# Kernel optimization log

Measured on AMD Instinct MI355X. Metric: run time of the kernel, lower is better.

The kernel has to match this reference:

```python
import jax, jax.numpy as jnp
import numpy as np

EPS = 1e-5
K = 20
LRELU = 0.2


def _bn(x, g, b, ch_axis):
    # inference BatchNorm with running_mean=0, running_var=1
    shape = [1] * x.ndim
    shape[ch_axis] = -1
    scale = (g / jnp.sqrt(1.0 + EPS)).reshape(shape)
    bias = b.reshape(shape)
    return x * scale + bias


def _lrelu(x):
    return jnp.where(x > 0, x, LRELU * x)


def _edge_conv(x, W, g, b):
    # x: (B, C, N) -> (B, C_out, N)
    B, C, N = x.shape
    xt = jnp.swapaxes(x, 1, 2)                      # (B, N, C)
    inner = -2.0 * jnp.einsum('bnc,bmc->bnm', xt, xt)
    xx = jnp.sum(xt * xt, axis=2)                   # (B, N)
    pdist = -xx[:, :, None] - inner - xx[:, None, :]  # negative sq dist (B,N,N)
    idx = jax.lax.top_k(pdist, K)[1]                # (B, N, K) nearest (incl. self)
    # gather neighbor features per batch: (C, N) indexed by (N, K) -> (C, N, K)
    neighbors = jax.vmap(lambda xf, id_: xf[:, id_])(x, idx)  # (B, C, N, K)
    center = jnp.broadcast_to(x[..., None], (B, C, N, K))
    edge = jnp.concatenate([center, neighbors - center], axis=1)  # (B, 2C, N, K)
    h = jnp.einsum('oc,bcnk->bonk', W, edge)        # 1x1 conv, no bias
    h = _lrelu(_bn(h, g, b, 1))
    return jnp.max(h, axis=-1)                      # (B, C_out, N)


def setup_inputs() -> dict:
    key = jax.random.key(0)
    ks = jax.random.split(key, 24)
    B, N = 4, 2048
    d = {}
    d['points'] = jax.random.normal(ks[0], (B, N, 3), dtype=jnp.float32)

    def w(k_, shape):
        return 0.1 * jax.random.normal(k_, shape, dtype=jnp.float32)

    def gam(k_, c):
        return 1.0 + 0.1 * jax.random.normal(k_, (c,), dtype=jnp.float32)

    def bet(k_, c):
        return 0.05 * jax.random.normal(k_, (c,), dtype=jnp.float32)

    # EdgeConv blocks: (out, 2*in)
    d['w1'], d['g1'], d['b1'] = w(ks[1], (64, 6)), gam(ks[2], 64), bet(ks[3], 64)
    d['w2'], d['g2'], d['b2'] = w(ks[4], (64, 128)), gam(ks[5], 64), bet(ks[6], 64)
    d['w3'], d['g3'], d['b3'] = w(ks[7], (128, 128)), gam(ks[8], 128), bet(ks[9], 128)
    d['w4'], d['g4'], d['b4'] = w(ks[10], (256, 256)), gam(ks[11], 256), bet(ks[12], 256)
    # conv5 1x1: 512 -> 1024
    d['w5'], d['g5'], d['b5'] = w(ks[13], (1024, 512)), gam(ks[14], 1024), bet(ks[15], 1024)
    # fc: 2048 -> 512 -> 256
    d['fw1'], d['fb1'] = w(ks[16], (512, 2048)), 0.05 * jax.random.normal(ks[17], (512,), dtype=jnp.float32)
    d['g6'], d['b6'] = gam(ks[18], 512), bet(ks[19], 512)
    d['fw2'], d['fb2'] = w(ks[20], (256, 512)), 0.05 * jax.random.normal(ks[21], (256,), dtype=jnp.float32)
    d['g7'], d['b7'] = gam(ks[22], 256), bet(ks[23], 256)
    return d


def reference(points, w1, g1, b1, w2, g2, b2, w3, g3, b3, w4, g4, b4,
              w5, g5, b5, fw1, fb1, g6, b6, fw2, fb2, g7, b7):
    x = jnp.swapaxes(points[:, :, :3], 1, 2)        # (B, 3, N)
    x1 = _edge_conv(x, w1, g1, b1)                  # (B, 64, N)
    x2 = _edge_conv(x1, w2, g2, b2)                 # (B, 64, N)
    x3 = _edge_conv(x2, w3, g3, b3)                 # (B, 128, N)
    x4 = _edge_conv(x3, w4, g4, b4)                 # (B, 256, N)
    h = jnp.concatenate([x1, x2, x3, x4], axis=1)   # (B, 512, N)
    h = _lrelu(_bn(jnp.einsum('oc,bcn->bon', w5, h), g5, b5, 1))  # (B, 1024, N)
    h_max = jnp.max(h, axis=-1)
    h_avg = jnp.mean(h, axis=-1)
    f = jnp.concatenate([h_max, h_avg], axis=1)     # (B, 2048)
    f = _lrelu(_bn(f @ fw1.T + fb1, g6, b6, 1))     # dropout = identity (eval)
    f = _bn(f @ fw2.T + fb2, g7, b7, 1)
    return f                                        # (B, 256)
```

## Files before the change

kernel.cpp:

```cpp
#include <hip/hip_runtime.h>
#include <hip/hip_bf16.h>
#include <float.h>

#define N_PTS 2048
#define B_SZ  4
#define KNN   20
#define LRELU_S 0.2f
#define FT    512
#define NPOOL 8

typedef __hip_bfloat16 bf16;
typedef __attribute__((ext_vector_type(8))) short short8v;
typedef __attribute__((ext_vector_type(4))) float floatx4;

__device__ __forceinline__ float b2f(const bf16 v) { return __bfloat162float(v); }
__device__ __forceinline__ float ldf(const float* p) { return *p; }
__device__ __forceinline__ float ldf(const bf16* p)  { return __bfloat162float(*p); }
__device__ __forceinline__ short8v ld8(const bf16* p) { return *(const short8v*)p; }
__device__ __forceinline__ unsigned umin(unsigned a, unsigned b) { return a < b ? a : b; }

__device__ __forceinline__ void gload16(const void* g, void* l) {
    __builtin_amdgcn_global_load_lds(
        (const __attribute__((address_space(1))) void*)g,
        (__attribute__((address_space(3))) void*)l, 16, 0, 0);
}

__global__ void k_sniff(const unsigned short* __restrict__ pts_hw, int* __restrict__ flag) {
    if (threadIdx.x != 0 || blockIdx.x != 0) return;
    int sane = 0;
    for (int j = 0; j < 64; ++j) {
        unsigned short v = pts_hw[2 * j];
        int e = (v >> 7) & 0xFF;
        if (e >= 100 && e <= 140) ++sane;
    }
    *flag = (sane >= 32) ? 1 : 0;
}

struct WPack {
    const void* src[23];
    int off[24];
    int rows[23];
    int cols[23];
};

__device__ __forceinline__ void repack_body(const WPack& wp, int isb,
                                            float* __restrict__ dst, int i, int limit) {
    if (i >= limit) return;
    int lo = 0, hi = 23;
    while (lo + 1 < hi) { int mid = (lo + hi) >> 1; if (i >= wp.off[mid]) lo = mid; else hi = mid; }
    int j = i - wp.off[lo];
    float v = isb ? b2f(((const bf16*)wp.src[lo])[j]) : ((const float*)wp.src[lo])[j];
    int dj = j;
    int cols = wp.cols[lo];
    if (cols) dj = (j % cols) * wp.rows[lo] + (j / cols);
    dst[wp.off[lo] + dj] = v;
}

template<int C, int COUT>
__device__ __forceinline__ void wsplit_body(const void* __restrict__ W, int isb,
                                            bf16* __restrict__ dst, int i) {
    if (i >= COUT * C) return;
    int o = i / C, c = i % C;
    float w1 = isb ? b2f(((const bf16*)W)[(size_t)o * 2 * C + c])
                   : ((const float*)W)[(size_t)o * 2 * C + c];
    float w2 = isb ? b2f(((const bf16*)W)[(size_t)o * 2 * C + C + c])
                   : ((const float*)W)[(size_t)o * 2 * C + C + c];
    float wd = w1 - w2;
    bf16 h2 = __float2bfloat16(w2);
    bf16 hd = __float2bfloat16(wd);
    dst[i]                = h2;
    dst[COUT * C + i]     = __float2bfloat16(w2 - b2f(h2));
    dst[2 * COUT * C + i] = hd;
    dst[3 * COUT * C + i] = __float2bfloat16(wd - b2f(hd));
}

__device__ __forceinline__ void w5split_body(const void* __restrict__ W, int isb,
                                             bf16* __restrict__ dst, int i) {
    if (i >= 1024 * 512) return;
    float w = isb ? b2f(((const bf16*)W)[i]) : ((const float*)W)[i];
    bf16 h = __float2bfloat16(w);
    dst[i] = h;
    dst[1024 * 512 + i] = __float2bfloat16(w - b2f(h));
}

__device__ __forceinline__ void transpose_body(const void* __restrict__ pts, int isb,
                                               float* __restrict__ x0, int i) {
    if (i >= B_SZ * N_PTS) return;
    int b = i / N_PTS, n = i % N_PTS;
    for (int c = 0; c < 3; ++c) {
        size_t s = ((size_t)b * N_PTS + n) * 3 + c;
        float v = isb ? b2f(((const bf16*)pts)[s]) : ((const float*)pts)[s];
        x0[((size_t)b * 3 + c) * N_PTS + n] = v;
    }
}

__global__ void k_prep(WPack wp, const int* __restrict__ flag, float* __restrict__ wf,
                       int rlimit,
                       const void* __restrict__ w2s, bf16* __restrict__ wsp2,
                       const void* __restrict__ w3s, bf16* __restrict__ wsp3,
                       const void* __restrict__ w4s, bf16* __restrict__ wsp4,
                       const void* __restrict__ w5s, bf16* __restrict__ w5sp,
                       const void* __restrict__ pts, float* __restrict__ x0) {
    const int isb = *flag;
    const int nbrep = (rlimit + 255) >> 8;
    int ib = blockIdx.x, t = threadIdx.x;
    if (ib < nbrep) { repack_body(wp, isb, wf, ib * 256 + t, rlimit); return; }
    ib -= nbrep;
    if (ib < 16)   { wsplit_body<64, 64>(w2s, isb, wsp2, ib * 256 + t); return; }
    ib -= 16;
    if (ib < 32)   { wsplit_body<64, 128>(w3s, isb, wsp3, ib * 256 + t); return; }
    ib -= 32;
    if (ib < 128)  { wsplit_body<128, 256>(w4s, isb, wsp4, ib * 256 + t); return; }
    ib -= 128;
    if (ib < 2048) { w5split_body(w5s, isb, w5sp, ib * 256 + t); return; }
    ib -= 2048;
    transpose_body(pts, isb, x0, ib * 256 + t);
}

__global__ void k_repack(WPack wp, const int* __restrict__ flag, float* __restrict__ dst, int limit) {
    repack_body(wp, *flag, dst, blockIdx.x * blockDim.x + threadIdx.x, limit);
}
__global__ void k_transpose(const void* __restrict__ pts, const int* __restrict__ flag,
                            float* __restrict__ x0) {
    transpose_body(pts, *flag, x0, blockIdx.x * blockDim.x + threadIdx.x);
}

__device__ __forceinline__ void load32(const float* row, int mbase, float* r) {
    const float4* p = (const float4*)(row + mbase);
#pragma unroll
    for (int i = 0; i < 8; ++i) {
        float4 f = p[i];
        r[4 * i + 0] = f.x; r[4 * i + 1] = f.y; r[4 * i + 2] = f.z; r[4 * i + 3] = f.w;
    }
}
__device__ __forceinline__ void load32(const bf16* row, int mbase, float* r) {
    const uint4* p = (const uint4*)(row + mbase);
// ... 67 lines not shown
        int q = threadIdx.x / 3, c = threadIdx.x % 3;
        qf[q][c] = xb[(size_t)c * N_PTS + q0 + q];
    }
    __syncthreads();

    int w = threadIdx.x >> 6, lane = threadIdx.x & 63;
    int qa = q0 + 2 * w;
    int mbase = lane * 32;

    float da[32], db[32];
#pragma unroll
    for (int j = 0; j < 32; ++j) { da[j] = 0.f; db[j] = 0.f; }
#pragma unroll
    for (int c = 0; c < 3; ++c) {
        float r[32];
        load32(xb + (size_t)c * N_PTS, mbase, r);
        float qac = qf[2 * w][c], qbc = qf[2 * w + 1][c];
#pragma unroll
        for (int j = 0; j < 32; ++j) {
            float ta = r[j] - qac; da[j] = fmaf(ta, ta, da[j]);
            float tb = r[j] - qbc; db[j] = fmaf(tb, tb, db[j]);
        }
    }
    unsigned ka[32], kb[32];
#pragma unroll
    for (int j = 0; j < 32; ++j) {
        ka[j] = (__float_as_uint(da[j]) & 0xFFFFF800u) | (unsigned)(mbase + j);
        kb[j] = (__float_as_uint(db[j]) & 0xFFFFF800u) | (unsigned)(mbase + j);
    }
    select20x2(ka, kb, idx + ((size_t)b * N_PTS + qa) * KNN,
               idx + ((size_t)b * N_PTS + qa + 1) * KNN, lane);
}

__global__ __launch_bounds__(256) void k_select2(const float* __restrict__ G,
                                                 const float* __restrict__ xx,
                                                 int* __restrict__ idx) {
    int ib = blockIdx.x;
    int b  = ib / (N_PTS / 8);
    int q0 = (ib % (N_PTS / 8)) * 8;
    int w = threadIdx.x >> 6, lane = threadIdx.x & 63;
    int qa = q0 + 2 * w;
    const float* gA = G + ((size_t)b * N_PTS + qa) * N_PTS;
    const float* gB = gA + N_PTS;
    const float* xr = xx + (size_t)b * N_PTS;
    float xqa = xr[qa], xqb = xr[qa + 1];

    unsigned ka[32], kb[32];
#pragma unroll
    for (int r = 0; r < 8; ++r) {
        int m0 = r * 256 + (lane << 2);
        float4 x4 = *(const float4*)(xr + m0);
        float4 a4 = *(const float4*)(gA + m0);
        float4 b4 = *(const float4*)(gB + m0);
        float s;
        s = fmaf(-2.f, a4.x, x4.x) + xqa; s = fmaxf(s, 0.f);
        ka[4 * r + 0] = (__float_as_uint(s) & 0xFFFFF800u) | (unsigned)(m0 + 0);
        s = fmaf(-2.f, a4.y, x4.y) + xqa; s = fmaxf(s, 0.f);
        ka[4 * r + 1] = (__float_as_uint(s) & 0xFFFFF800u) | (unsigned)(m0 + 1);
        s = fmaf(-2.f, a4.z, x4.z) + xqa; s = fmaxf(s, 0.f);
        ka[4 * r + 2] = (__float_as_uint(s) & 0xFFFFF800u) | (unsigned)(m0 + 2);
        s = fmaf(-2.f, a4.w, x4.w) + xqa; s = fmaxf(s, 0.f);
        ka[4 * r + 3] = (__float_as_uint(s) & 0xFFFFF800u) | (unsigned)(m0 + 3);
        s = fmaf(-2.f, b4.x, x4.x) + xqb; s = fmaxf(s, 0.f);
        kb[4 * r + 0] = (__float_as_uint(s) & 0xFFFFF800u) | (unsigned)(m0 + 0);
        s = fmaf(-2.f, b4.y, x4.y) + xqb; s = fmaxf(s, 0.f);
        kb[4 * r + 1] = (__float_as_uint(s) & 0xFFFFF800u) | (unsigned)(m0 + 1);
        s = fmaf(-2.f, b4.z, x4.z) + xqb; s = fmaxf(s, 0.f);
        kb[4 * r + 2] = (__float_as_uint(s) & 0xFFFFF800u) | (unsigned)(m0 + 2);
        s = fmaf(-2.f, b4.w, x4.w) + xqb; s = fmaxf(s, 0.f);
        kb[4 * r + 3] = (__float_as_uint(s) & 0xFFFFF800u) | (unsigned)(m0 + 3);
    }
    select20x2(ka, kb, idx + ((size_t)b * N_PTS + qa) * KNN,
               idx + ((size_t)b * N_PTS + qa + 1) * KNN, lane);
}

template<typename T, int C>
__global__ __launch_bounds__(256) void k_knn(const T* __restrict__ x, int bstride,
                                             int* __restrict__ idx) {
    __shared__ float qf[4][C];
    int ib = blockIdx.x;
    int b  = ib / (N_PTS / 4);
    int q0 = (ib % (N_PTS / 4)) * 4;
    const T* xb = x + (size_t)b * bstride;

    for (int t = threadIdx.x; t < 4 * C; t += 256) {
        int pt = t / C, c = t % C;
        qf[pt][c] = ldf(&xb[(size_t)c * N_PTS + (q0 + pt)]);
    }
    __syncthreads();

    int w = threadIdx.x >> 6, lane = threadIdx.x & 63;
    int q = q0 + w;
    int mbase = lane * 32;

    float v[32];
#pragma unroll
    for (int j = 0; j < 32; ++j) v[j] = 0.f;

    for (int c = 0; c < C; ++c) {
        float qc = qf[w][c];
        float r[32];
        load32(xb + (size_t)c * N_PTS, mbase, r);
#pragma unroll
        for (int j = 0; j < 32; ++j) { float t = r[j] - qc; v[j] = fmaf(t, t, v[j]); }
    }

    for (int k = 0; k < KNN; ++k) {
        float bv = FLT_MAX; int bi = 0x7FFFFFFF;
#pragma unroll
        for (int j = 0; j < 32; ++j)
            if (v[j] < bv) { bv = v[j]; bi = mbase + j; }
#pragma unroll
        for (int off = 32; off >= 1; off >>= 1) {
            float ov = __shfl_xor(bv, off);
            int   oi = __shfl_xor(bi, off);
            if (ov < bv || (ov == bv && oi < bi)) { bv = ov; bi = oi; }
        }
        if (lane == 0) idx[((size_t)b * N_PTS + q) * KNN + k] = bi;
        int wl = bi >> 5, wj = bi & 31;
        if (lane == wl) {
#pragma unroll
            for (int j = 0; j < 32; ++j) if (j == wj) v[j] = FLT_MAX;
        }
    }
}

template<int C>
__global__ __launch_bounds__(256) void k_gram(const bf16* __restrict__ featT, int c0,
                                              float* __restrict__ G) {
    const int KC = 64;
    __shared__ __align__(16) short At[128 * 64];
    __shared__ __align__(16) short Bt[128 * 64];

    int ib = blockIdx.x;
    int b  = ib >> 8;
    int t  = ib & 255;
    int n0 = (t >> 4) << 7;
    int m0 = (t & 15) << 7;

    int tid = threadIdx.x;
    int w = tid >> 6, lane = tid & 63;
    int rw = (w & 1) * 64, cw = (w >> 1) * 64;
    int lrow = lane & 15, quad = lane >> 4;

    floatx4 acc[4][4];
#pragma unroll
    for (int ri = 0; ri < 4; ++ri)
#pragma unroll
        for (int ci = 0; ci < 4; ++ci) acc[ri][ci] = (floatx4){0.f, 0.f, 0.f, 0.f};

    for (int ck = 0; ck < C; ck += KC) {
        __syncthreads();
#pragma unroll
        for (int it = 0; it < 4; ++it) {
            int s = tid + it * 256;
            int row = s >> 3, seg = s & 7;
            int gseg = seg ^ (row & 7);
            gload16(featT + ((size_t)(b * N_PTS + n0 + row) * FT) + c0 + ck + gseg * 8,
                    &At[(s & ~63) * 8]);
            gload16(featT + ((size_t)(b * N_PTS + m0 + row) * FT) + c0 + ck + gseg * 8,
                    &Bt[(s & ~63) * 8]);
        }
        __syncthreads();
#pragma unroll
        for (int kk = 0; kk < KC; kk += 32) {
            int ks = kk >> 3;
            short8v a[4], bb[4];
#pragma unroll
            for (int ri = 0; ri < 4; ++ri) {
                int row = rw + ri * 16 + lrow;
                int seg = (ks + quad) ^ (row & 7);
                a[ri] = *(const short8v*)&At[row * 64 + seg * 8];
            }
#pragma unroll
            for (int ci = 0; ci < 4; ++ci) {
                int row = cw + ci * 16 + lrow;
                int seg = (ks + quad) ^ (row & 7);
                bb[ci] = *(const short8v*)&Bt[row * 64 + seg * 8];
            }
#pragma unroll
            for (int ri = 0; ri < 4; ++ri)
#pragma unroll
                for (int ci = 0; ci < 4; ++ci)
                    acc[ri][ci] = __builtin_amdgcn_mfma_f32_16x16x32_bf16(a[ri], bb[ci], acc[ri][ci], 0, 0, 0);
        }
    }

#pragma unroll
    for (int ri = 0; ri < 4; ++ri)
#pragma unroll
        for (int ci = 0; ci < 4; ++ci) {
            int n = n0 + rw + ri * 16 + quad * 4;
            int m = m0 + cw + ci * 16 + lrow;
            float* gp = G + ((size_t)b * N_PTS + n) * N_PTS + m;
#pragma unroll
            for (int reg = 0; reg < 4; ++reg)
                gp[(size_t)reg * N_PTS] = acc[ri][ci][reg];
        }
}

template<int COUT, int C>
__global__ __launch_bounds__(256) void k_xform(const bf16* __restrict__ featT, int c0,
                                               const bf16* __restrict__ Wsp,
                                               float* __restrict__ Y,
                                               const int* __restrict__ flag) {
    const int M2 = 2 * COUT;
    const int KC = 64;
    __shared__ __align__(16) short Bt[128 * 64];

    const int isb = *flag;
    int ib = blockIdx.x;
    int nt = ib & 63;
    int mt = ib >> 6;
    int tid = threadIdx.x;
    int w = tid >> 6, lane = tid & 63;
    int rw = (w & 1) * 64, cw = (w >> 1) * 64;
    int l15 = lane & 15, quad = lane >> 4;

    floatx4 acc[4][4];
#pragma unroll
    for (int ri = 0; ri < 4; ++ri)
#pragma unroll
        for (int ci = 0; ci < 4; ++ci) acc[ri][ci] = (floatx4){0.f, 0.f, 0.f, 0.f};

    for (int ck = 0; ck < C; ck += KC) {
        __syncthreads();
#pragma unroll
        for (int it = 0; it < 4; ++it) {
            int s = tid + it * 256;
            int row = s >> 3, seg = s & 7;
            int gseg = seg ^ (row & 7);
            gload16(featT + (size_t)(nt * 128 + row) * FT + c0 + ck + gseg * 8,
                    &Bt[(s & ~63) * 8]);
        }
        __syncthreads();
#pragma unroll
        for (int kk = 0; kk < KC; kk += 32) {
            int ks = kk >> 3;
            short8v bfr[4];
#pragma unroll
            for (int ci = 0; ci < 4; ++ci) {
                int row = cw + ci * 16 + l15;
                int seg = (ks + quad) ^ (row & 7);
                bfr[ci] = *(const short8v*)&Bt[row * 64 + seg * 8];
            }
#pragma unroll
            for (int ri = 0; ri < 4; ++ri) {
                int rbase = mt * 128 + rw + ri * 16;
                bool uselo = (!isb) || (rbase >= COUT);
                int mrow = rbase + l15;
                int base = (mrow < COUT) ? mrow : (mrow + COUT);
                const bf16* hi = Wsp + (size_t)base * C + ck + kk + quad * 8;
                short8v ah = ld8(hi);
                short8v al;
                if (uselo) al = ld8(hi + (size_t)COUT * C);
#pragma unroll
                for (int ci = 0; ci < 4; ++ci) {
                    acc[ri][ci] = __builtin_amdgcn_mfma_f32_16x16x32_bf16(ah, bfr[ci], acc[ri][ci], 0, 0, 0);
                    if (uselo)
                        acc[ri][ci] = __builtin_amdgcn_mfma_f32_16x16x32_bf16(al, bfr[ci], acc[ri][ci], 0, 0, 0);
                }
            }
        }
    }

#pragma unroll
    for (int ri = 0; ri < 4; ++ri)
#pragma unroll
        for (int ci = 0; ci < 4; ++ci) {
            int n = nt * 128 + cw + ci * 16 + l15;
            int m = mt * 128 + rw + ri * 16 + quad * 4;
            *(floatx4*)(Y + (size_t)n * M2 + m) = acc[ri][ci];
        }
}

template<int COUT>
__global__ __launch_bounds__(256) void k_gmax(const float* __restrict__ Y,
        const int* __restrict__ idx,
        const float* __restrict__ gam, const float* __restrict__ bet,
        bf16* __restrict__ featT, int c0f, float* __restrict__ xxout) {
    const int M2 = 2 * COUT;
    const int OT = COUT / 64;
    int i = blockIdx.x * 4 + (threadIdx.x >> 6);
    int lane = threadIdx.x & 63;
    int b = i >> 11;

    const float inv = rsqrtf(1.0f + 1e-5f);
    float yd[OT], scale[OT], bias[OT], mx[OT];
#pragma unroll
    for (int j = 0; j < OT; ++j) {
        int o = lane + 64 * j;
        yd[j]    = Y[(size_t)i * M2 + COUT + o];
        scale[j] = gam[o] * inv;
        bias[j]  = bet[o];
        mx[j]    = -FLT_MAX;
    }

    const int* ip = idx + (size_t)i * KNN;
    const float* Yb = Y + ((size_t)b * N_PTS) * M2;
#pragma unroll 4
    for (int k = 0; k < KNN; ++k) {
        int m = ip[k] & (N_PTS - 1);
        const float* yr = Yb + (size_t)m * M2;
#pragma unroll
        for (int j = 0; j < OT; ++j) {
            float h = (yd[j] + yr[lane + 64 * j]) * scale[j] + bias[j];
            h = h > 0.f ? h : LRELU_S * h;
            mx[j] = fmaxf(mx[j], h);
        }
    }
    float s = 0.f;
#pragma unroll
    for (int j = 0; j < OT; ++j) {
        bf16 bv = __float2bfloat16(mx[j]);
        featT[(size_t)i * FT + c0f + lane + 64 * j] = bv;
        if (xxout) { float q = b2f(bv); s = fmaf(q, q, s); }
    }
    if (xxout) {
#pragma unroll
        for (int off = 32; off >= 1; off >>= 1) s += __shfl_xor(s, off);
        if (lane == 0) xxout[i] = s;
    }
}

template<typename T, int C, int COUT, bool WF>
__global__ __launch_bounds__(256) void k_edgeconv(const T* __restrict__ x, int bstride,
                           const int* __restrict__ idx,
                           const float* __restrict__ Wt,
                           const float* __restrict__ gam,
                           const float* __restrict__ bet,
                           bf16* __restrict__ out, int ostride,
                           bf16* __restrict__ featT, int c0f,
                           float* __restrict__ xxout) {
    const int PT = 4;
    const int OT = COUT / 64;
    const int CP = (C + 3) & ~3;
    __shared__ float sh[PT][KNN + 1][CP];

    int ib = blockIdx.x;
    int b  = ib / (N_PTS / PT);
    int n0 = (ib % (N_PTS / PT)) * PT;
    const T* xb = x + (size_t)b * bstride;

    const int TOT = PT * (KNN + 1) * C;
    for (int t = threadIdx.x; t < TOT; t += 256) {
        int pt = t / ((KNN + 1) * C);
        int r  = t % ((KNN + 1) * C);
        int row = r / C, c = r % C;
        int n = n0 + pt;
        int m = (row == 0) ? n
                           : (idx[((size_t)b * N_PTS + n) * KNN + (row - 1)] & (N_PTS - 1));
        sh[pt][row][c] = ldf(&xb[(size_t)c * N_PTS + m]);
    }
    __syncthreads();
// ... 28 lines not shown
            if (pass == 0) {
#pragma unroll
                for (int j = 0; j < OT; ++j) {
                    float w1v = Wt[(size_t)c * COUT + lane + 64 * j];
                    base[j] = fmaf(w1v - w2v[j], xq, base[j]);
                }
            }
#pragma unroll
            for (int k = 0; k < KT; ++k) {
                float nv = sh[w][1 + pass * KT + k][c];
#pragma unroll
                for (int j = 0; j < OT; ++j) acc[j][k] = fmaf(w2v[j], nv, acc[j][k]);
            }
        }

#pragma unroll
        for (int j = 0; j < OT; ++j) {
            int o = lane + 64 * j;
            float scale = gam[o] * inv, bias = bet[o];
#pragma unroll
            for (int k = 0; k < KT; ++k) {
                float h = (base[j] + acc[j][k]) * scale + bias;
                h = h > 0.f ? h : LRELU_S * h;
                mx[j] = fmaxf(mx[j], h);
            }
        }
    }

    float s = 0.f;
#pragma unroll
    for (int j = 0; j < OT; ++j) {
        int o = lane + 64 * j;
        bf16 bv = __float2bfloat16(mx[j]);
        out[(size_t)b * ostride + (size_t)o * N_PTS + n] = bv;
        if (WF) {
            featT[((size_t)b * N_PTS + n) * FT + c0f + o] = bv;
            float q = b2f(bv);
            s = fmaf(q, q, s);
        }
    }
    if (WF && xxout) {
#pragma unroll
        for (int off = 32; off >= 1; off >>= 1) s += __shfl_xor(s, off);
        if (lane == 0) xxout[(size_t)b * N_PTS + n] = s;
    }
}

__global__ __launch_bounds__(256) void k_conv5mfma(
        const bf16* __restrict__ featT, const bf16* __restrict__ w5sp,
        const float* __restrict__ g5, const float* __restrict__ b5,
        float* __restrict__ fmxp, float* __restrict__ fsmp,
        const int* __restrict__ flag) {
    __shared__ __align__(16) short Bt[256 * 64];
    __shared__ __align__(16) short Ah[64 * 64];
    __shared__ __align__(16) short Al[64 * 64];
    __shared__ float rmx[4][64];
    __shared__ float rsm[4][64];

    const int isb = *flag;
    int ib = blockIdx.x;
    int b  = ib / 128;
    int rem = ib % 128;
    int o0 = (rem >> 3) * 64;
    int nt = rem & 7;
    int tid = threadIdx.x;
    int w = tid >> 6, lane = tid & 63;
    int l15 = lane & 15, quad = lane >> 4;
// ... 302 lines not shown
extern "C" void kernel_launch(void* const* d_in, const int* in_sizes, int n_in,
                              void* d_out, int out_size, void* d_ws, size_t ws_size,
                              hipStream_t stream) {
    static const int wsz[23] = {
        384, 64, 64,   8192, 64, 64,   16384, 128, 128,   65536, 256, 256,
        524288, 1024, 1024,   1048576, 512,   512, 512,   131072, 256,   256, 256
    };
    static const int trows[23] = {64,0,0, 64,0,0, 128,0,0, 256,0,0, 0,0,0, 0,0, 0,0, 0,0, 0,0};
    static const int tcols[23] = { 6,0,0,128,0,0, 128,0,0, 256,0,0, 0,0,0, 0,0, 0,0, 0,0, 0,0};

    WPack wp;
    int total = 0;
    for (int i = 0; i < 23; ++i) {
        wp.src[i] = d_in[i + 1]; wp.off[i] = total; total += wsz[i];
        wp.rows[i] = trows[i]; wp.cols[i] = tcols[i];
    }
    wp.off[23] = total;

    const size_t flag_bytes = 16;
    const size_t x0_bytes   = (size_t)B_SZ * 3 * N_PTS * 4;
    const size_t feat_bytes = (size_t)B_SZ * 512 * N_PTS * 2;
    const size_t idx_bytes  = (size_t)B_SZ * N_PTS * KNN * 4;
    const size_t pool_bytes = (size_t)B_SZ * 1024 * 4 * 2;
    const size_t wf_bytes   = (size_t)total * 4;
    const size_t base_need  = flag_bytes + x0_bytes + feat_bytes + idx_bytes + pool_bytes + wf_bytes;

    const size_t featT_bytes = (size_t)B_SZ * N_PTS * FT * 2;
    const size_t xx_bytes    = (size_t)B_SZ * N_PTS * 4;
    const size_t wsp2_elems  = 4 * 64 * 64;
    const size_t wsp3_elems  = 4 * 128 * 64;
    const size_t wsp4_elems  = 4 * 256 * 128;
    const size_t w5sp_elems  = 2 * 1024 * 512;
    const size_t wsp_bytes   = (wsp2_elems + wsp3_elems + wsp4_elems + w5sp_elems) * 2;
    const size_t S_bytes     = (size_t)B_SZ * N_PTS * N_PTS * 4;
    const size_t full_need   = base_need + featT_bytes + xx_bytes + wsp_bytes + S_bytes;

    if (ws_size < base_need) return;
    const bool use_gram = (ws_size >= full_need);

    char* w = (char*)d_ws;
    int*   flag = (int*)w;              w += flag_bytes;
    float* x0   = (float*)w;            w += x0_bytes;
    bf16*  feat = (bf16*)w;             w += feat_bytes;
    int*   idx  = (int*)w;              w += idx_bytes;
    w += pool_bytes;
    float* wf   = (float*)w;            w += wf_bytes;
    bf16*  featT = (bf16*)w;            w += featT_bytes;
    float* xx    = (float*)w;           w += xx_bytes;
    bf16*  wsp2  = (bf16*)w;            w += wsp2_elems * 2;
    bf16*  wsp3  = (bf16*)w;            w += wsp3_elems * 2;
    bf16*  wsp4  = (bf16*)w;            w += wsp4_elems * 2;
    bf16*  w5sp  = (bf16*)w;            w += w5sp_elems * 2;
    float* S     = (float*)w;

    float* fmxp = (float*)idx;
    float* fsmp = fmxp + (size_t)B_SZ * 1024 * NPOOL;
    float* fvec = fsmp + (size_t)B_SZ * 1024 * NPOOL;
    float* tbuf = fvec + (size_t)B_SZ * 2048;

    const int FBS = 512 * N_PTS;

    k_sniff<<<1, 64, 0, stream>>>((const unsigned short*)d_in[0], flag);

    const float* w1t = wf + wp.off[0],  *g1 = wf + wp.off[1],  *b1 = wf + wp.off[2];
    const float* w2t = wf + wp.off[3],  *g2 = wf + wp.off[4],  *b2 = wf + wp.off[5];
    const float* w3t = wf + wp.off[6],  *g3 = wf + wp.off[7],  *b3 = wf + wp.off[8];
    const float* w4t = wf + wp.off[9],  *g4 = wf + wp.off[10], *b4 = wf + wp.off[11];
    const float* w5  = wf + wp.off[12], *g5 = wf + wp.off[13], *b5 = wf + wp.off[14];
    const float* fw1 = wf + wp.off[15], *fb1 = wf + wp.off[16];
    const float* g6  = wf + wp.off[17], *b6 = wf + wp.off[18];
    const float* fw2 = wf + wp.off[19], *fb2 = wf + wp.off[20];
    const float* g7  = wf + wp.off[21], *b7 = wf + wp.off[22];

    const int GK = B_SZ * N_PTS / 4;
    const int G8 = B_SZ * N_PTS / 8;

    if (use_gram) {
        const int rlimit = wp.off[15];
        const int nbrep = (rlimit + 255) / 256;
        const int prep_grid = nbrep + 16 + 32 + 128 + 2048 + 32;
        k_prep<<<prep_grid, 256, 0, stream>>>(wp, flag, wf, rlimit,
                                              d_in[4], wsp2, d_in[7], wsp3,
                                              d_in[10], wsp4, d_in[13], w5sp,
                                              d_in[0], x0);

        k_knn3<<<G8, 256, 0, stream>>>(x0, idx);
        k_edgeconv<float, 3, 64, true><<<GK, 256, 0, stream>>>(
            x0, 3 * N_PTS, idx, w1t, g1, b1, feat + 0 * N_PTS, FBS, featT, 0, xx);
        k_gram<64><<<B_SZ * 256, 256, 0, stream>>>(featT, 0, S);
        k_select2<<<G8, 256, 0, stream>>>(S, xx, idx);
        k_xform<64, 64><<<64, 256, 0, stream>>>(featT, 0, wsp2, S, flag);
        k_gmax<64><<<GK, 256, 0, stream>>>(S, idx, g2, b2, featT, 64, xx);
        k_gram<64><<<B_SZ * 256, 256, 0, stream>>>(featT, 64, S);
        k_select2<<<G8, 256, 0, stream>>>(S, xx, idx);
        k_xform<128, 64><<<128, 256, 0, stream>>>(featT, 64, wsp3, S, flag);
        k_gmax<128><<<GK, 256, 0, stream>>>(S, idx, g3, b3, featT, 128, xx);
        k_gram<128><<<B_SZ * 256, 256, 0, stream>>>(featT, 128, S);
        k_select2<<<G8, 256, 0, stream>>>(S, xx, idx);
        k_xform<256, 128><<<256, 256, 0, stream>>>(featT, 128, wsp4, S, flag);
        k_gmax<256><<<GK, 256, 0, stream>>>(S, idx, g4, b4, featT, 256, nullptr);

        k_conv5mfma<<<B_SZ * 128, 256, 0, stream>>>(featT, w5sp, g5, b5, fmxp, fsmp, flag);
        k_pool<<<(B_SZ * 1024 + 255) / 256, 256, 0, stream>>>(fmxp, fsmp, fvec);
        k_fc1<<<B_SZ * 512, 256, 0, stream>>>(fvec, d_in[16], d_in[17], d_in[18], d_in[19],
                                              flag, tbuf);
        k_fc2<<<B_SZ * 256, 256, 0, stream>>>(tbuf, d_in[20], d_in[21], d_in[22], d_in[23],
                                              flag, d_out);
    } else {
        k_repack<<<(total + 255) / 256, 256, 0, stream>>>(wp, flag, wf, total);
        k_transpose<<<(B_SZ * N_PTS + 255) / 256, 256, 0, stream>>>(d_in[0], flag, x0);

        k_knn<float, 3><<<GK, 256, 0, stream>>>(x0, 3 * N_PTS, idx);
        k_edgeconv<float, 3, 64, false><<<GK, 256, 0, stream>>>(
            x0, 3 * N_PTS, idx, w1t, g1, b1, feat + 0 * N_PTS, FBS, nullptr, 0, nullptr);
        k_knn<bf16, 64><<<GK, 256, 0, stream>>>(feat + 0 * N_PTS, FBS, idx);
        k_edgeconv<bf16, 64, 64, false><<<GK, 256, 0, stream>>>(
            feat + 0 * N_PTS, FBS, idx, w2t, g2, b2, feat + 64 * N_PTS, FBS, nullptr, 0, nullptr);
        k_knn<bf16, 64><<<GK, 256, 0, stream>>>(feat + 64 * N_PTS, FBS, idx);
        k_edgeconv<bf16, 64, 128, false><<<GK, 256, 0, stream>>>(
            feat + 64 * N_PTS, FBS, idx, w3t, g3, b3, feat + 128 * N_PTS, FBS, nullptr, 0, nullptr);
        k_knn<bf16, 128><<<GK, 256, 0, stream>>>(feat + 128 * N_PTS, FBS, idx);
        k_edgeconv<bf16, 128, 256, false><<<GK, 256, 0, stream>>>(
            feat + 128 * N_PTS, FBS, idx, w4t, g4, b4, feat + 256 * N_PTS, FBS, nullptr, 0, nullptr);

        k_conv5pool<<<B_SZ * (1024 / 8) * NCH, 256, 0, stream>>>(feat, w5, g5, b5, fmxp, fsmp);
        k_head<<<B_SZ, 256, 0, stream>>>(fmxp, fsmp, fw1, fb1, g6, b6, fw2, fb2, g7, b7,
                                         flag, d_out);
    }
}
```

Before: 382.2 us.

## Fuse gram with xform and kNN select with neighbor max; store Y in bf16

Each of the three later EdgeConv stages now runs in two launches instead of four. The gram and feature-transform GEMMs share one launch. The top-k selection feeds its neighbor indices through shared memory straight into the gather-max, so the idx buffer is no longer written and read back in global memory. The transformed features Y are stored as bf16 in a separate buffer instead of fp32 in S. This cuts gather traffic but adds rounding error. The sniff kernel is folded into k_prep and edgeconv1 skips its redundant channel-major write, which removes more launches and writes. The xx buffers are double-buffered to avoid read/write hazards.

```diff
diff --git a/kernel.cpp b/kernel.cpp
--- a/kernel.cpp
+++ b/kernel.cpp
@@ -11,6 +11,7 @@
 
 typedef __hip_bfloat16 bf16;
 typedef __attribute__((ext_vector_type(8))) short short8v;
+typedef __attribute__((ext_vector_type(4))) short short4v;
 typedef __attribute__((ext_vector_type(4))) float floatx4;
 
 __device__ __forceinline__ float b2f(const bf16 v) { return __bfloat162float(v); }
@@ -18,6 +19,10 @@
 __device__ __forceinline__ float ldf(const bf16* p)  { return __bfloat162float(*p); }
 __device__ __forceinline__ short8v ld8(const bf16* p) { return *(const short8v*)p; }
 __device__ __forceinline__ unsigned umin(unsigned a, unsigned b) { return a < b ? a : b; }
+__device__ __forceinline__ short bfbits(float f) {
+    bf16 t = __float2bfloat16(f);
+    return *reinterpret_cast<short*>(&t);
+}
 
 __device__ __forceinline__ void gload16(const void* g, void* l) {
     __builtin_amdgcn_global_load_lds(
@@ -25,15 +30,19 @@
         (__attribute__((address_space(3))) void*)l, 16, 0, 0);
 }
 
-__global__ void k_sniff(const unsigned short* __restrict__ pts_hw, int* __restrict__ flag) {
-    if (threadIdx.x != 0 || blockIdx.x != 0) return;
+__device__ __forceinline__ int sniff_body(const unsigned short* pts_hw) {
     int sane = 0;
     for (int j = 0; j < 64; ++j) {
         unsigned short v = pts_hw[2 * j];
         int e = (v >> 7) & 0xFF;
         if (e >= 100 && e <= 140) ++sane;
     }
-    *flag = (sane >= 32) ? 1 : 0;
+    return (sane >= 32) ? 1 : 0;
+}
+
+__global__ void k_sniff(const unsigned short* __restrict__ pts_hw, int* __restrict__ flag) {
+    if (threadIdx.x != 0 || blockIdx.x != 0) return;
+    *flag = sniff_body(pts_hw);
 }
 
 struct WPack {
@@ -94,14 +103,21 @@
     }
 }
 
-__global__ void k_prep(WPack wp, const int* __restrict__ flag, float* __restrict__ wf,
-                       int rlimit,
+__global__ void k_prep(WPack wp, float* __restrict__ wf, int rlimit,
                        const void* __restrict__ w2s, bf16* __restrict__ wsp2,
                        const void* __restrict__ w3s, bf16* __restrict__ wsp3,
                        const void* __restrict__ w4s, bf16* __restrict__ wsp4,
                        const void* __restrict__ w5s, bf16* __restrict__ w5sp,
-                       const void* __restrict__ pts, float* __restrict__ x0) {
-    const int isb = *flag;
+                       const void* __restrict__ pts, float* __restrict__ x0,
+                       int* __restrict__ flagout) {
+    __shared__ int sfl;
+    if (threadIdx.x == 0) {
+        int f = sniff_body((const unsigned short*)pts);
+        sfl = f;
+        if (blockIdx.x == 0) *flagout = f;
+    }
+    __syncthreads();
+    const int isb = sfl;
     const int nbrep = (rlimit + 255) >> 8;
     int ib = blockIdx.x, t = threadIdx.x;
     if (ib < nbrep) { repack_body(wp, isb, wf, ib * 256 + t, rlimit); return; }
@@ -235,9 +251,226 @@
                idx + ((size_t)b * N_PTS + qa + 1) * KNN, lane);
 }
 
-__global__ __launch_bounds__(256) void k_select2(const float* __restrict__ G,
-                                                 const float* __restrict__ xx,
-                                                 int* __restrict__ idx) {
+template<typename T, int C>
+__global__ __launch_bounds__(256) void k_knn(const T* __restrict__ x, int bstride,
+                                             int* __restrict__ idx) {
+    __shared__ float qf[4][C];
+    int ib = blockIdx.x;
+    int b  = ib / (N_PTS / 4);
+    int q0 = (ib % (N_PTS / 4)) * 4;
+    const T* xb = x + (size_t)b * bstride;
+
+    for (int t = threadIdx.x; t < 4 * C; t += 256) {
+        int pt = t / C, c = t % C;
+        qf[pt][c] = ldf(&xb[(size_t)c * N_PTS + (q0 + pt)]);
+    }
+    __syncthreads();
+
+    int w = threadIdx.x >> 6, lane = threadIdx.x & 63;
+    int q = q0 + w;
+    int mbase = lane * 32;
+
+    float v[32];
+#pragma unroll
+    for (int j = 0; j < 32; ++j) v[j] = 0.f;
+
+    for (int c = 0; c < C; ++c) {
+        float qc = qf[w][c];
+        float r[32];
+        load32(xb + (size_t)c * N_PTS, mbase, r);
+#pragma unroll
+        for (int j = 0; j < 32; ++j) { float t = r[j] - qc; v[j] = fmaf(t, t, v[j]); }
+    }
+
+    for (int k = 0; k < KNN; ++k) {
+        float bv = FLT_MAX; int bi = 0x7FFFFFFF;
+#pragma unroll
+        for (int j = 0; j < 32; ++j)
+            if (v[j] < bv) { bv = v[j]; bi = mbase + j; }
+#pragma unroll
+        for (int off = 32; off >= 1; off >>= 1) {
+            float ov = __shfl_xor(bv, off);
+            int   oi = __shfl_xor(bi, off);
+            if (ov < bv || (ov == bv && oi < bi)) { bv = ov; bi = oi; }
+        }
+        if (lane == 0) idx[((size_t)b * N_PTS + q) * KNN + k] = bi;
+        int wl = bi >> 5, wj = bi & 31;
+        if (lane == wl) {
+#pragma unroll
+            for (int j = 0; j < 32; ++j) if (j == wj) v[j] = FLT_MAX;
+        }
+    }
+}
+
+template<int C>
+__device__ __forceinline__ void gram_body(const bf16* __restrict__ featT, int c0,
+                                          float* __restrict__ G,
+                                          short* At, short* Bt, int ib) {
+    const int KC = 64;
+    int b  = ib >> 8;
+    int t  = ib & 255;
+    int n0 = (t >> 4) << 7;
+    int m0 = (t & 15) << 7;
+
+    int tid = threadIdx.x;
+    int w = tid >> 6, lane = tid & 63;
+    int rw = (w & 1) * 64, cw = (w >> 1) * 64;
+    int lrow = lane & 15, quad = lane >> 4;
+
+    floatx4 acc[4][4];
+#pragma unroll
+    for (int ri = 0; ri < 4; ++ri)
+#pragma unroll
+        for (int ci = 0; ci < 4; ++ci) acc[ri][ci] = (floatx4){0.f, 0.f, 0.f, 0.f};
+
+    for (int ck = 0; ck < C; ck += KC) {
+        __syncthreads();
+#pragma unroll
+        for (int it = 0; it < 4; ++it) {
+            int s = tid + it * 256;
+            int row = s >> 3, seg = s & 7;
+            int gseg = seg ^ (row & 7);
+            gload16(featT + ((size_t)(b * N_PTS + n0 + row) * FT) + c0 + ck + gseg * 8,
+                    &At[(s & ~63) * 8]);
+            gload16(featT + ((size_t)(b * N_PTS + m0 + row) * FT) + c0 + ck + gseg * 8,
+                    &Bt[(s & ~63) * 8]);
+        }
+        __syncthreads();
+#pragma unroll
+        for (int kk = 0; kk < KC; kk += 32) {
+            int ks = kk >> 3;
+            short8v a[4], bb[4];
+#pragma unroll
+            for (int ri = 0; ri < 4; ++ri) {
+                int row = rw + ri * 16 + lrow;
+                int seg = (ks + quad) ^ (row & 7);
+                a[ri] = *(const short8v*)&At[row * 64 + seg * 8];
+            }
+#pragma unroll
+            for (int ci = 0; ci < 4; ++ci) {
+                int row = cw + ci * 16 + lrow;
+                int seg = (ks + quad) ^ (row & 7);
+                bb[ci] = *(const short8v*)&Bt[row * 64 + seg * 8];
+            }
+#pragma unroll
+            for (int ri = 0; ri < 4; ++ri)
+#pragma unroll
+                for (int ci = 0; ci < 4; ++ci)
+                    acc[ri][ci] = __builtin_amdgcn_mfma_f32_16x16x32_bf16(a[ri], bb[ci], acc[ri][ci], 0, 0, 0);
+        }
+    }
+
+#pragma unroll
+    for (int ri = 0; ri < 4; ++ri)
+#pragma unroll
+        for (int ci = 0; ci < 4; ++ci) {
+            int n = n0 + rw + ri * 16 + quad * 4;
+            int m = m0 + cw + ci * 16 + lrow;
+            float* gp = G + ((size_t)b * N_PTS + n) * N_PTS + m;
+#pragma unroll
+            for (int reg = 0; reg < 4; ++reg)
+                gp[(size_t)reg * N_PTS] = acc[ri][ci][reg];
+        }
+}
+
+template<int COUT, int C>
+__device__ __forceinline__ void xform_body(const bf16* __restrict__ featT, int c0,
+                                           const bf16* __restrict__ Wsp,
+                                           bf16* __restrict__ Yh, int isb,
+                                           short* Bt, int ib2) {
+    const int M2 = 2 * COUT;
+    const int KC = 64;
+    int nt = ib2 & 63;
+    int mt = ib2 >> 6;
+    int tid = threadIdx.x;
+    int w = tid >> 6, lane = tid & 63;
+    int rw = (w & 1) * 64, cw = (w >> 1) * 64;
+    int l15 = lane & 15, quad = lane >> 4;
+
+    floatx4 acc[4][4];
+#pragma unroll
+    for (int ri = 0; ri < 4; ++ri)
+#pragma unroll
+        for (int ci = 0; ci < 4; ++ci) acc[ri][ci] = (floatx4){0.f, 0.f, 0.f, 0.f};
+
+    for (int ck = 0; ck < C; ck += KC) {
+        __syncthreads();
+#pragma unroll
+        for (int it = 0; it < 4; ++it) {
+            int s = tid + it * 256;
+            int row = s >> 3, seg = s & 7;
+            int gseg = seg ^ (row & 7);
+            gload16(featT + (size_t)(nt * 128 + row) * FT + c0 + ck + gseg * 8,
+                    &Bt[(s & ~63) * 8]);
+        }
+        __syncthreads();
+#pragma unroll
+        for (int kk = 0; kk < KC; kk += 32) {
+            int ks = kk >> 3;
+            short8v bfr[4];
+#pragma unroll
+            for (int ci = 0; ci < 4; ++ci) {
+                int row = cw + ci * 16 + l15;
+                int seg = (ks + quad) ^ (row & 7);
+                bfr[ci] = *(const short8v*)&Bt[row * 64 + seg * 8];
+            }
+#pragma unroll
+            for (int ri = 0; ri < 4; ++ri) {
+                int rbase = mt * 128 + rw + ri * 16;
+                bool uselo = (!isb) || (rbase >= COUT);
+                int mrow = rbase + l15;
+                int base = (mrow < COUT) ? mrow : (mrow + COUT);
+                const bf16* hi = Wsp + (size_t)base * C + ck + kk + quad * 8;
+                short8v ah = ld8(hi);
+                short8v al;
+                if (uselo) al = ld8(hi + (size_t)COUT * C);
+#pragma unroll
+                for (int ci = 0; ci < 4; ++ci) {
+                    acc[ri][ci] = __builtin_amdgcn_mfma_f32_16x16x32_bf16(ah, bfr[ci], acc[ri][ci], 0, 0, 0);
+                    if (uselo)
+                        acc[ri][ci] = __builtin_amdgcn_mfma_f32_16x16x32_bf16(al, bfr[ci], acc[ri][ci], 0, 0, 0);
+                }
+            }
+        }
+    }
+
+#pragma unroll
+    for (int ri = 0; ri < 4; ++ri)
+#pragma unroll
+        for (int ci = 0; ci < 4; ++ci) {
+            int n = nt * 128 + cw + ci * 16 + l15;
+            int m = mt * 128 + rw + ri * 16 + quad * 4;
+            short4v o4;
+            o4[0] = bfbits(acc[ri][ci][0]);
+            o4[1] = bfbits(acc[ri][ci][1]);
+            o4[2] = bfbits(acc[ri][ci][2]);
+            o4[3] = bfbits(acc[ri][ci][3]);
+            *(short4v*)(Yh + (size_t)n * M2 + m) = o4;
+        }
+}
+
+template<int C, int COUT>
+__global__ __launch_bounds__(256) void k_gx(const bf16* __restrict__ featT, int c0,
+        const bf16* __restrict__ Wsp, float* __restrict__ G, bf16* __restrict__ Yh,
+        const int* __restrict__ flag) {
+    __shared__ __align__(16) short lds[2 * 128 * 64];
+    int ib = blockIdx.x;
+    if (ib < B_SZ * 256) {
+        gram_body<C>(featT, c0, G, lds, lds + 128 * 64, ib);
+    } else {
+        xform_body<COUT, C>(featT, c0, Wsp, Yh, *flag, lds, ib - B_SZ * 256);
+    }
+}
+
+template<int COUT>
+__global__ __launch_bounds__(256) void k_selgmax(const float* __restrict__ G,
+        const float* __restrict__ xxin, const bf16* __restrict__ Yh,
+        const float* __restrict__ gam, const float* __restrict__ bet,
+        bf16* __restrict__ featT, int c0f, float* __restrict__ xxout) {
+    const int M2 = 2 * COUT;
+    const int OT = COUT / 64;
+    __shared__ int sidx[8][KNN];
+
     int ib = blockIdx.x;
     int b  = ib / (N_PTS / 8);
     int q0 = (ib % (N_PTS / 8)) * 8;
@@ -245,7 +478,7 @@
     int qa = q0 + 2 * w;
     const float* gA = G + ((size_t)b * N_PTS + qa) * N_PTS;
     const float* gB = gA + N_PTS;
-    const float* xr = xx + (size_t)b * N_PTS;
+    const float* xr = xxin + (size_t)b * N_PTS;
     float xqa = xr[qa], xqb = xr[qa + 1];
 
     unsigned ka[32], kb[32];
@@ -273,256 +506,58 @@
         s = fmaf(-2.f, b4.w, x4.w) + xqb; s = fmaxf(s, 0.f);
         kb[4 * r + 3] = (__float_as_uint(s) & 0xFFFFF800u) | (unsigned)(m0 + 3);
     }
-    select20x2(ka, kb, idx + ((size_t)b * N_PTS + qa) * KNN,
-               idx + ((size_t)b * N_PTS + qa + 1) * KNN, lane);
-}
-
-template<typename T, int C>
-__global__ __launch_bounds__(256) void k_knn(const T* __restrict__ x, int bstride,
-                                             int* __restrict__ idx) {
-    __shared__ float qf[4][C];
-    int ib = blockIdx.x;
-    int b  = ib / (N_PTS / 4);
-    int q0 = (ib % (N_PTS / 4)) * 4;
-    const T* xb = x + (size_t)b * bstride;
-
-    for (int t = threadIdx.x; t < 4 * C; t += 256) {
-        int pt = t / C, c = t % C;
-        qf[pt][c] = ldf(&xb[(size_t)c * N_PTS + (q0 + pt)]);
-    }
+    select20x2(ka, kb, &sidx[2 * w][0], &sidx[2 * w + 1][0], lane);
     __syncthreads();
 
-    int w = threadIdx.x >> 6, lane = threadIdx.x & 63;
-    int q = q0 + w;
-    int mbase = lane * 32;
-
-    float v[32];
-#pragma unroll
-    for (int j = 0; j < 32; ++j) v[j] = 0.f;
-
-    for (int c = 0; c < C; ++c) {
-        float qc = qf[w][c];
-        float r[32];
-        load32(xb + (size_t)c * N_PTS, mbase, r);
-#pragma unroll
-        for (int j = 0; j < 32; ++j) { float t = r[j] - qc; v[j] = fmaf(t, t, v[j]); }
-    }
-
-    for (int k = 0; k < KNN; ++k) {
-        float bv = FLT_MAX; int bi = 0x7FFFFFFF;
-#pragma unroll
-        for (int j = 0; j < 32; ++j)
-            if (v[j] < bv) { bv = v[j]; bi = mbase + j; }
-#pragma unroll
-        for (int off = 32; off >= 1; off >>= 1) {
-            float ov = __shfl_xor(bv, off);
-            int   oi = __shfl_xor(bi, off);
-            if (ov < bv || (ov == bv && oi < bi)) { bv = ov; bi = oi; }
-        }
-        if (lane == 0) idx[((size_t)b * N_PTS + q) * KNN + k] = bi;
-        int wl = bi >> 5, wj = bi & 31;
-        if (lane == wl) {
-#pragma unroll
-            for (int j = 0; j < 32; ++j) if (j == wj) v[j] = FLT_MAX;
-        }
-    }
-}
-
-template<int C>
-__global__ __launch_bounds__(256) void k_gram(const bf16* __restrict__ featT, int c0,
-                                              float* __restrict__ G) {
-    const int KC = 64;
-    __shared__ __align__(16) short At[128 * 64];
-    __shared__ __align__(16) short Bt[128 * 64];
-
-    int ib = blockIdx.x;
-    int b  = ib >> 8;
-    int t  = ib & 255;
-    int n0 = (t >> 4) << 7;
-    int m0 = (t & 15) << 7;
-
-    int tid = threadIdx.x;
-    int w = tid >> 6, lane = tid & 63;
-    int rw = (w & 1) * 64, cw = (w >> 1) * 64;
-    int lrow = lane & 15, quad = lane >> 4;
-
-    floatx4 acc[4][4];
-#pragma unroll
-    for (int ri = 0; ri < 4; ++ri)
-#pragma unroll
-        for (int ci = 0; ci < 4; ++ci) acc[ri][ci] = (floatx4){0.f, 0.f, 0.f, 0.f};
-
-    for (int ck = 0; ck < C; ck += KC) {
-        __syncthreads();
-#pragma unroll
-        for (int it = 0; it < 4; ++it) {
-            int s = tid + it * 256;
-            int row = s >> 3, seg = s & 7;
-            int gseg = seg ^ (row & 7);
-            gload16(featT + ((size_t)(b * N_PTS + n0 + row) * FT) + c0 + ck + gseg * 8,
-                    &At[(s & ~63) * 8]);
-            gload16(featT + ((size_t)(b * N_PTS + m0 + row) * FT) + c0 + ck + gseg * 8,
-                    &Bt[(s & ~63) * 8]);
-        }
-        __syncthreads();
-#pragma unroll
-        for (int kk = 0; kk < KC; kk += 32) {
-            int ks = kk >> 3;
-            short8v a[4], bb[4];
-#pragma unroll
-            for (int ri = 0; ri < 4; ++ri) {
-                int row = rw + ri * 16 + lrow;
-                int seg = (ks + quad) ^ (row & 7);
-                a[ri] = *(const short8v*)&At[row * 64 + seg * 8];
-            }
-#pragma unroll
-            for (int ci = 0; ci < 4; ++ci) {
-                int row = cw + ci * 16 + lrow;
-                int seg = (ks + quad) ^ (row & 7);
-                bb[ci] = *(const short8v*)&Bt[row * 64 + seg * 8];
-            }
-#pragma unroll
-            for (int ri = 0; ri < 4; ++ri)
-#pragma unroll
-                for (int ci = 0; ci < 4; ++ci)
-                    acc[ri][ci] = __builtin_amdgcn_mfma_f32_16x16x32_bf16(a[ri], bb[ci], acc[ri][ci], 0, 0, 0);
-        }
-    }
-
-#pragma unroll
-    for (int ri = 0; ri < 4; ++ri)
-#pragma unroll
-        for (int ci = 0; ci < 4; ++ci) {
-            int n = n0 + rw + ri * 16 + quad * 4;
-            int m = m0 + cw + ci * 16 + lrow;
-            float* gp = G + ((size_t)b * N_PTS + n) * N_PTS + m;
-#pragma unroll
-            for (int reg = 0; reg < 4; ++reg)
-                gp[(size_t)reg * N_PTS] = acc[ri][ci][reg];
-        }
-}
-
-template<int COUT, int C>
-__global__ __launch_bounds__(256) void k_xform(const bf16* __restrict__ featT, int c0,
-                                               const bf16* __restrict__ Wsp,
-                                               float* __restrict__ Y,
-                                               const int* __restrict__ flag) {
-    const int M2 = 2 * COUT;
-    const int KC = 64;
-    __shared__ __align__(16) short Bt[128 * 64];
-
-    const int isb = *flag;
-    int ib = blockIdx.x;
-    int nt = ib & 63;
-    int mt = ib >> 6;
-    int tid = threadIdx.x;
-    int w = tid >> 6, lane = tid & 63;
-    int rw = (w & 1) * 64, cw = (w >> 1) * 64;
-    int l15 = lane & 15, quad = lane >> 4;
-
-    floatx4 acc[4][4];
-#pragma unroll
-    for (int ri = 0; ri < 4; ++ri)
-#pragma unroll
-        for (int ci = 0; ci < 4; ++ci) acc[ri][ci] = (floatx4){0.f, 0.f, 0.f, 0.f};
-
-    for (int ck = 0; ck < C; ck += KC) {
-        __syncthreads();
-#pragma unroll
-        for (int it = 0; it < 4; ++it) {
-            int s = tid + it * 256;
-            int row = s >> 3, seg = s & 7;
-            int gseg = seg ^ (row & 7);
-            gload16(featT + (size_t)(nt * 128 + row) * FT + c0 + ck + gseg * 8,
-                    &Bt[(s & ~63) * 8]);
-        }
-        __syncthreads();
-#pragma unroll
-        for (int kk = 0; kk < KC; kk += 32) {
-            int ks = kk >> 3;
-            short8v bfr[4];
-#pragma unroll
-            for (int ci = 0; ci < 4; ++ci) {
-                int row = cw + ci * 16 + l15;
-                int seg = (ks + quad) ^ (row & 7);
-                bfr[ci] = *(const short8v*)&Bt[row * 64 + seg * 8];
-            }
-#pragma unroll
-            for (int ri = 0; ri < 4; ++ri) {
-                int rbase = mt * 128 + rw + ri * 16;
-                bool uselo = (!isb) || (rbase >= COUT);
-                int mrow = rbase + l15;
-                int base = (mrow < COUT) ? mrow : (mrow + COUT);
-                const bf16* hi = Wsp + (size_t)base * C + ck + kk + quad * 8;
-                short8v ah = ld8(hi);
-                short8v al;
-                if (uselo) al = ld8(hi + (size_t)COUT * C);
-#pragma unroll
-                for (int ci = 0; ci < 4; ++ci) {
-                    acc[ri][ci] = __builtin_amdgcn_mfma_f32_16x16x32_bf16(ah, bfr[ci], acc[ri][ci], 0, 0, 0);
-                    if (uselo)
-                        acc[ri][ci] = __builtin_amdgcn_mfma_f32_16x16x32_bf16(al, bfr[ci], acc[ri][ci], 0, 0, 0);
-                }
-            }
-        }
-    }
-
-#pragma unroll
-    for (int ri = 0; ri < 4; ++ri)
-#pragma unroll
-        for (int ci = 0; ci < 4; ++ci) {
-            int n = nt * 128 + cw + ci * 16 + l15;
-            int m = mt * 128 + rw + ri * 16 + quad * 4;
-            *(floatx4*)(Y + (size_t)n * M2 + m) = acc[ri][ci];
-        }
-}
-
-template<int COUT>
-__global__ __launch_bounds__(256) void k_gmax(const float* __restrict__ Y,
-        const int* __restrict__ idx,
-        const float* __restrict__ gam, const float* __restrict__ bet,
-        bf16* __restrict__ featT, int c0f, float* __restrict__ xxout) {
-    const int M2 = 2 * COUT;
-    const int OT = COUT / 64;
-    int i = blockIdx.x * 4 + (threadIdx.x >> 6);
-    int lane = threadIdx.x & 63;
-    int b = i >> 11;
-
+    size_t iA = (size_t)b * N_PTS + qa;
     const float inv = rsqrtf(1.0f + 1e-5f);
-    float yd[OT], scale[OT], bias[OT], mx[OT];
+    float yda[OT], ydb[OT], scl[OT], bis[OT], mxa[OT], mxb[OT];
 #pragma unroll
     for (int j = 0; j < OT; ++j) {
         int o = lane + 64 * j;
-        yd[j]    = Y[(size_t)i * M2 + COUT + o];
-        scale[j] = gam[o] * inv;
-        bias[j]  = bet[o];
-        mx[j]    = -FLT_MAX;
-    }
-
-    const int* ip = idx + (size_t)i * KNN;
-    const float* Yb = Y + ((size_t)b * N_PTS) * M2;
-#pragma unroll 4
+        yda[j] = b2f(Yh[iA * M2 + COUT + o]);
+        ydb[j] = b2f(Yh[(iA + 1) * M2 + COUT + o]);
+        scl[j] = gam[o] * inv;
+        bis[j] = bet[o];
+        mxa[j] = -FLT_MAX; mxb[j] = -FLT_MAX;
+    }
+    const bf16* Yb = Yh + (size_t)b * N_PTS * M2;
+#pragma unroll
     for (int k = 0; k < KNN; ++k) {
-        int m = ip[k] & (N_PTS - 1);
-        const float* yr = Yb + (size_t)m * M2;
+        int m0 = sidx[2 * w][k] & (N_PTS - 1);
+        int m1 = sidx[2 * w + 1][k] & (N_PTS - 1);
+        const bf16* r0 = Yb + (size_t)m0 * M2;
+        const bf16* r1 = Yb + (size_t)m1 * M2;
 #pragma unroll
         for (int j = 0; j < OT; ++j) {
-            float h = (yd[j] + yr[lane + 64 * j]) * scale[j] + bias[j];
-            h = h > 0.f ? h : LRELU_S * h;
-            mx[j] = fmaxf(mx[j], h);
-        }
-    }
-    float s = 0.f;
+            int o = lane + 64 * j;
+            float ha = (yda[j] + b2f(r0[o])) * scl[j] + bis[j];
+            ha = ha > 0.f ? ha : LRELU_S * ha;
+            mxa[j] = fmaxf(mxa[j], ha);
+            float hb = (ydb[j] + b2f(r1[o])) * scl[j] + bis[j];
+            hb = hb > 0.f ? hb : LRELU_S * hb;
+            mxb[j] = fmaxf(mxb[j], hb);
+        }
+    }
+    float sa = 0.f, sb = 0.f;
 #pragma unroll
     for (int j = 0; j < OT; ++j) {
-        bf16 bv = __float2bfloat16(mx[j]);
-        featT[(size_t)i * FT + c0f + lane + 64 * j] = bv;
-        if (xxout) { float q = b2f(bv); s = fmaf(q, q, s); }
+        bf16 va = __float2bfloat16(mxa[j]);
+        bf16 vb = __float2bfloat16(mxb[j]);
+        featT[iA * FT + c0f + lane + 64 * j] = va;
+        featT[(iA + 1) * FT + c0f + lane + 64 * j] = vb;
+        if (xxout) {
+            float pa = b2f(va); sa = fmaf(pa, pa, sa);
+            float pb = b2f(vb); sb = fmaf(pb, pb, sb);
+        }
     }
     if (xxout) {
 #pragma unroll
-        for (int off = 32; off >= 1; off >>= 1) s += __shfl_xor(s, off);
-        if (lane == 0) xxout[i] = s;
+        for (int off = 32; off >= 1; off >>= 1) {
+            sa += __shfl_xor(sa, off);
+            sb += __shfl_xor(sb, off);
+        }
+        if (lane == 0) { xxout[iA] = sa; xxout[iA + 1] = sb; }
     }
 }
 
@@ -617,7 +652,7 @@
     for (int j = 0; j < OT; ++j) {
         int o = lane + 64 * j;
         bf16 bv = __float2bfloat16(mx[j]);
-        out[(size_t)b * ostride + (size_t)o * N_PTS + n] = bv;
+        if (!WF) out[(size_t)b * ostride + (size_t)o * N_PTS + n] = bv;
         if (WF) {
             featT[((size_t)b * N_PTS + n) * FT + c0f + o] = bv;
             float q = b2f(bv);
@@ -986,8 +1021,10 @@
     const size_t wsp4_elems  = 4 * 256 * 128;
     const size_t w5sp_elems  = 2 * 1024 * 512;
     const size_t wsp_bytes   = (wsp2_elems + wsp3_elems + wsp4_elems + w5sp_elems) * 2;
+    const size_t Yh_bytes    = (size_t)B_SZ * N_PTS * 512 * 2;
     const size_t S_bytes     = (size_t)B_SZ * N_PTS * N_PTS * 4;
-    const size_t full_need   = base_need + featT_bytes + xx_bytes + wsp_bytes + S_bytes;
+    const size_t full_need   = base_need + featT_bytes + 2 * xx_bytes + wsp_bytes
+                             + Yh_bytes + S_bytes;
 
     if (ws_size < base_need) return;
     const bool use_gram = (ws_size >= full_need);
@@ -1000,11 +1037,13 @@
     w += pool_bytes;
     float* wf   = (float*)w;            w += wf_bytes;
     bf16*  featT = (bf16*)w;            w += featT_bytes;
-    float* xx    = (float*)w;           w += xx_bytes;
+    float* xxA   = (float*)w;           w += xx_bytes;
+    float* xxB   = (float*)w;           w += xx_bytes;
     bf16*  wsp2  = (bf16*)w;            w += wsp2_elems * 2;
     bf16*  wsp3  = (bf16*)w;            w += wsp3_elems * 2;
     bf16*  wsp4  = (bf16*)w;            w += wsp4_elems * 2;
     bf16*  w5sp  = (bf16*)w;            w += w5sp_elems * 2;
+    bf16*  Yh    = (bf16*)w;            w += Yh_bytes;
     float* S     = (float*)w;
 
     float* fmxp = (float*)idx;
@@ -1013,8 +1052,6 @@
     float* tbuf = fvec + (size_t)B_SZ * 2048;
 
     const int FBS = 512 * N_PTS;
-
-    k_sniff<<<1, 64, 0, stream>>>((const unsigned short*)d_in[0], flag);
 
     const float* w1t = wf + wp.off[0],  *g1 = wf + wp.off[1],  *b1 = wf + wp.off[2];
     const float* w2t = wf + wp.off[3],  *g2 = wf + wp.off[4],  *b2 = wf + wp.off[5];
@@ -1028,31 +1065,26 @@
 
     const int GK = B_SZ * N_PTS / 4;
     const int G8 = B_SZ * N_PTS / 8;
+    const int NG = B_SZ * 256;
 
     if (use_gram) {
         const int rlimit = wp.off[15];
         const int nbrep = (rlimit + 255) / 256;
         const int prep_grid = nbrep + 16 + 32 + 128 + 2048 + 32;
-        k_prep<<<prep_grid, 256, 0, stream>>>(wp, flag, wf, rlimit,
+        k_prep<<<prep_grid, 256, 0, stream>>>(wp, wf, rlimit,
                                               d_in[4], wsp2, d_in[7], wsp3,
                                               d_in[10], wsp4, d_in[13], w5sp,
-                                              d_in[0], x0);
+                                              d_in[0], x0, flag);
 
         k_knn3<<<G8, 256, 0, stream>>>(x0, idx);
         k_edgeconv<float, 3, 64, true><<<GK, 256, 0, stream>>>(
-            x0, 3 * N_PTS, idx, w1t, g1, b1, feat + 0 * N_PTS, FBS, featT, 0, xx);
-        k_gram<64><<<B_SZ * 256, 256, 0, stream>>>(featT, 0, S);
-        k_select2<<<G8, 256, 0, stream>>>(S, xx, idx);
-        k_xform<64, 64><<<64, 256, 0, stream>>>(featT, 0, wsp2, S, flag);
-        k_gmax<64><<<GK, 256, 0, stream>>>(S, idx, g2, b2, featT, 64, xx);
-        k_gram<64><<<B_SZ * 256, 256, 0, stream>>>(featT, 64, S);
-        k_select2<<<G8, 256, 0, stream>>>(S, xx, idx);
-        k_xform<128, 64><<<128, 256, 0, stream>>>(featT, 64, wsp3, S, flag);
-        k_gmax<128><<<GK, 256, 0, stream>>>(S, idx, g3, b3, featT, 128, xx);
-        k_gram<128><<<B_SZ * 256, 256, 0, stream>>>(featT, 128, S);
-        k_select2<<<G8, 256, 0, stream>>>(S, xx, idx);
-        k_xform<256, 128><<<256, 256, 0, stream>>>(featT, 128, wsp4, S, flag);
-        k_gmax<256><<<GK, 256, 0, stream>>>(S, idx, g4, b4, featT, 256, nullptr);
+            x0, 3 * N_PTS, idx, w1t, g1, b1, feat, FBS, featT, 0, xxA);
+        k_gx<64, 64><<<NG + 64, 256, 0, stream>>>(featT, 0, wsp2, S, Yh, flag);
+        k_selgmax<64><<<G8, 256, 0, stream>>>(S, xxA, Yh, g2, b2, featT, 64, xxB);
+        k_gx<64, 128><<<NG + 128, 256, 0, stream>>>(featT, 64, wsp3, S, Yh, flag);
+        k_selgmax<128><<<G8, 256, 0, stream>>>(S, xxB, Yh, g3, b3, featT, 128, xxA);
+        k_gx<128, 256><<<NG + 256, 256, 0, stream>>>(featT, 128, wsp4, S, Yh, flag);
+        k_selgmax<256><<<G8, 256, 0, stream>>>(S, xxA, Yh, g4, b4, featT, 256, nullptr);
 
         k_conv5mfma<<<B_SZ * 128, 256, 0, stream>>>(featT, w5sp, g5, b5, fmxp, fsmp, flag);
         k_pool<<<(B_SZ * 1024 + 255) / 256, 256, 0, stream>>>(fmxp, fsmp, fvec);
@@ -1061,6 +1093,7 @@
         k_fc2<<<B_SZ * 256, 256, 0, stream>>>(tbuf, d_in[20], d_in[21], d_in[22], d_in[23],
                                               flag, d_out);
     } else {
+        k_sniff<<<1, 64, 0, stream>>>((const unsigned short*)d_in[0], flag);
         k_repack<<<(total + 255) / 256, 256, 0, stream>>>(wp, flag, wf, total);
         k_transpose<<<(B_SZ * N_PTS + 255) / 256, 256, 0, stream>>>(d_in[0], flag, x0);
 
```

Measured after the change: 350.7 us. 8.2% less time.
